# Kernel optimization log

Measured on AMD Instinct MI355X. Metric: run time of the kernel, lower is better.

Reference implementation:

```python
import jax, jax.numpy as jnp
from jax import lax
import numpy as np
import math

EPS = 1e-6

def _np(a, s=1.0):
    return np.asarray(a, dtype=np.float32) * np.float32(s)

def _gabor(theta, sigma=1.1, lambd=3.0, gamma=0.65):
    c = np.arange(-2, 3, dtype=np.float32)
    yy, xx = np.meshgrid(c, c, indexing='ij')
    xt = xx * math.cos(theta) + yy * math.sin(theta)
    yt = -xx * math.sin(theta) + yy * math.cos(theta)
    k = np.exp(-(xt**2 + gamma**2 * yt**2) / (2.0 * sigma**2)) * np.cos(2.0 * math.pi * xt / lambd)
    k = k - k.mean()
    return (k / max(np.abs(k).sum(), 1e-6)).astype(np.float32)

def _dct_like(u=2, v=2, size=5):
    c = np.arange(size, dtype=np.float32)
    yy, xx = np.meshgrid(c, c, indexing='ij')
    k = np.cos(math.pi*(2*xx+1)*u/(2*size)) * np.cos(math.pi*(2*yy+1)*v/(2*size))
    k = k - k.mean()
    return (k / max(np.abs(k).sum(), 1e-6)).astype(np.float32)

# stacked 3x3 stencils: laplacian, hess_xx, hess_yy, hess_xy, sobel_x, sobel_y, diag_main, diag_anti, checkerboard
_K3 = np.stack([
    _np([[0,1,0],[1,-4,1],[0,1,0]]),
    _np([[0,0,0],[1,-2,1],[0,0,0]]),
    _np([[0,1,0],[0,-2,0],[0,1,0]]),
    _np([[1,0,-1],[0,0,0],[-1,0,1]], 0.25),
    _np([[-1,0,1],[-2,0,2],[-1,0,1]], 0.125),
    _np([[-1,-2,-1],[0,0,0],[1,2,1]], 0.125),
    _np([[-2,-1,0],[-1,0,1],[0,1,2]], 0.125),
    _np([[0,1,2],[-1,0,1],[-2,-1,0]], 0.125),
    _np([[1,-1,1],[-1,1,-1],[1,-1,1]], 1.0/9.0),
])[:, None]

_Z5 = np.zeros((5,5), np.float32)

def _row5(vals):
    k = _Z5.copy(); k[2, :] = vals; return k

def _col5(vals):
    k = _Z5.copy(); k[:, 2] = vals; return k

# stacked 5x5 stencils: ha_second_h, ha_second_v, ha_green_h, ha_green_v, mhc_green, stripe_x, stripe_y, gabor45, gabor135, dct
_K5 = np.stack([
    _row5([-0.5, 0.0, 1.0, 0.0, -0.5]),
    _col5([-0.5, 0.0, 1.0, 0.0, -0.5]),
    _row5([-0.25, 0.5, 0.5, 0.5, -0.25]),
    _col5([-0.25, 0.5, 0.5, 0.5, -0.25]),
    _np([[0,0,-1,0,0],[0,0,2,0,0],[-1,2,4,2,-1],[0,0,2,0,0],[0,0,-1,0,0]], 0.125),
    _row5([0.25, -1.0, 1.5, -1.0, 0.25]),
    _col5([0.25, -1.0, 1.5, -1.0, 0.25]),
    _gabor(math.pi/4.0),
    _gabor(3.0*math.pi/4.0),
    _dct_like(),
])[:, None]

_SMOOTH5 = (_np([[1,2,3,2,1],[2,4,6,4,2],[3,6,9,6,3],[2,4,6,4,2],[1,2,3,2,1]]) / np.float32(81.0))[None, None]

K3 = jnp.asarray(_K3)
K5 = jnp.asarray(_K5)
SMOOTH5 = jnp.asarray(_SMOOTH5)

def _masks(H, W):
    # gbrg pattern
    z = lambda: np.zeros((1, 1, H, W), np.float32)
    r, b, gr, gb, row, col = z(), z(), z(), z(), z(), z()
    row[:, :, 1::2, :] = 1.0
    col[:, :, :, 1::2] = 1.0
    gb[:, :, 0::2, 0::2] = 1.0
    b[:, :, 0::2, 1::2] = 1.0
    r[:, :, 1::2, 0::2] = 1.0
    gr[:, :, 1::2, 1::2] = 1.0
    g = gr + gb
    return tuple(jnp.asarray(a) for a in (r, g, b, gr, gb, row, col))

def _pad(x, ph, pw):
    return jnp.pad(x, ((0, 0), (0, 0), (ph, ph), (pw, pw)), mode='reflect')

def _conv_same(x, k, groups=1):
    kh, kw = k.shape[-2:]
    return lax.conv_general_dilated(_pad(x, kh // 2, kw // 2), k.astype(x.dtype), (1, 1), 'VALID',
                                    dimension_numbers=('NCHW', 'OIHW', 'NCHW'),
                                    feature_group_count=groups)

def _avg_same(x, kh, kw):
    k = jnp.full((1, 1, kh, kw), 1.0 / (kh * kw), x.dtype)
    return _conv_same(x, k)

def _forward(bayer):
    B, _, H, W = bayer.shape
    r, g, b, gr, gb, row, col = _masks(H, W)
    c3 = _conv_same(bayer, K3)  # [B,9,H,W]
    lap, hxx, hyy, hxy, gx, gy, gdm, gda, chk = jnp.split(c3, 9, axis=1)
    c5 = _conv_same(bayer, K5)  # [B,10,H,W]
    hsh, hsv, hgh, hgv, mhcf, stx, sty, g45, g135, dctp = jnp.split(c5, 10, axis=1)
    # morphological gradient: 3x3 max - min (reflect-padded)
    xp = _pad(bayer, 1, 1)
    mgrad = (lax.reduce_window(xp, -jnp.inf, lax.max, (1, 1, 3, 3), (1, 1, 1, 1), 'VALID')
             - lax.reduce_window(xp, jnp.inf, lax.min, (1, 1, 3, 3), (1, 1, 1, 1), 'VALID'))
    gmag = jnp.sqrt(gx * gx + gy * gy + EPS)
    # structure tensor (3x3 box smoothing of gradient outer products)
    jxx = _avg_same(gx * gx, 3, 3)
    jyy = _avg_same(gy * gy, 3, 3)
    jxy = _avg_same(gx * gy, 3, 3)
    tr = jxx + jyy
    lam_gap = jnp.sqrt((jxx - jyy) ** 2 + 4.0 * jxy * jxy + EPS)
    coherence = lam_gap / (tr + EPS)
    anisotropy = (jxx - jyy) / (tr + EPS)
    ha_dis = jnp.abs(hgh - hgv)
    res_h = bayer - hgh
    res_v = bayer - hgv
    res_eh = _avg_same(res_h * res_h, 3, 3)
    res_ev = _avg_same(res_v * res_v, 3, 3)
    dgd = jnp.abs(gx) - jnp.abs(gy)
    dsd = jnp.abs(hxx) - jnp.abs(hyy)
    # 1x5 / 5x1 line variances
    mh = _avg_same(bayer, 1, 5)
    mv = _avg_same(bayer, 5, 1)
    lvh = jnp.maximum(_avg_same(bayer * bayer, 1, 5) - mh * mh, 0.0)
    lvv = jnp.maximum(_avg_same(bayer * bayer, 5, 1) - mv * mv, 0.0)
    lvd = lvh - lvv
    dconf = jnp.abs(lvd) / (lvh + lvv + EPS)
    # normalized sparse fills (smooth5 of masked signal / smooth5 of mask)
    mstack = jnp.concatenate([r, g, b, gr, gb], axis=1)  # [1,5,H,W]
    sig = bayer * mstack  # [B,5,H,W]
    ks = jnp.tile(SMOOTH5, (5, 1, 1, 1))
    num = _conv_same(sig, ks, groups=5)
    den = jnp.maximum(_conv_same(mstack, ks, groups=5), EPS)
    rf, gf, bf, grf, gbf = jnp.split(num / den, 5, axis=1)
    rg = rf - gf
    bg = bf - gf
    gpd = grf - gbf
    mhc = jnp.where(g > 0.5, bayer, mhcf)
    mhc_ha = mhc - 0.5 * (hgh + hgv)
    rres = (bayer - mhc) * r
    bres = (bayer - mhc) * b
    chk_e = _avg_same(chk * chk, 3, 3)
    str_e = _avg_same(stx * stx + sty * sty, 3, 3)
    lmean = _avg_same(bayer, 3, 3)
    lvar = jnp.maximum(_avg_same(bayer * bayer, 3, 3) - lmean * lmean, 0.0)
    gen = _avg_same(gx * gx + gy * gy, 3, 3)
    bm = lambda m: jnp.broadcast_to(m, bayer.shape)
    feats = [bm(r), bm(g), bm(b), bm(gr), bm(gb), bm(row), bm(col),
             lap, hxx, hyy, hxy, mgrad, gx, gy, gdm, gda, gmag,
             coherence, anisotropy, hsh, hsv, hgh, hgv, ha_dis,
             res_h, res_v, res_eh, res_ev, dgd, dsd, lvh, lvv, lvd, dconf,
             rg, bg, gpd, mhc, mhc_ha, rres, bres,
             stx, sty, chk, g45, g135, dctp, chk_e, str_e, lmean, lvar, gen]
    return jnp.concatenate(feats, axis=1)  # [B,52,H,W]

def setup_inputs() -> dict:
    key = jax.random.key(0)
    bayer = jax.random.uniform(key, (2, 1, 768, 768), dtype=jnp.float32)
    return {"bayer": bayer}

def reference(bayer):
    return _forward(bayer)
```

## Files before the change

### kernel.cpp

```cpp
#include <hip/hip_runtime.h>
#include <math.h>

#define H_ 768
#define W_ 768
#define TY 16
#define TX 64
#define NTHREADS 256
#define EPS_ 1e-6f

typedef float f4 __attribute__((ext_vector_type(4)));

__device__ __forceinline__ f4 mk4(float x, float y, float z, float w){ f4 r; r.x=x; r.y=y; r.z=z; r.w=w; return r; }
__device__ __forceinline__ f4 sp(float s){ return mk4(s,s,s,s); }
__device__ __forceinline__ f4 max4(f4 a, f4 b){ return mk4(fmaxf(a.x,b.x),fmaxf(a.y,b.y),fmaxf(a.z,b.z),fmaxf(a.w,b.w)); }
__device__ __forceinline__ f4 min4(f4 a, f4 b){ return mk4(fminf(a.x,b.x),fminf(a.y,b.y),fminf(a.z,b.z),fminf(a.w,b.w)); }
__device__ __forceinline__ f4 sqrt4(f4 a){ return mk4(sqrtf(a.x),sqrtf(a.y),sqrtf(a.z),sqrtf(a.w)); }
__device__ __forceinline__ f4 abs4(f4 a){ return mk4(fabsf(a.x),fabsf(a.y),fabsf(a.z),fabsf(a.w)); }
__device__ __forceinline__ float rcp1(float x){
#if __has_builtin(__builtin_amdgcn_rcpf)
    return __builtin_amdgcn_rcpf(x);
#else
    return 1.0f / x;
#endif
}
__device__ __forceinline__ f4 rcp4(f4 a){ return mk4(rcp1(a.x),rcp1(a.y),rcp1(a.z),rcp1(a.w)); }

__device__ __forceinline__ int refl(int c, int n) {
    c = c < 0 ? -c : c;
    return c >= n ? 2 * n - 2 - c : c;
}

__global__ __launch_bounds__(NTHREADS, 4)
void bayer_feat(const float* __restrict__ in, float* __restrict__ out) {
    const int bz  = blockIdx.z;
    const int gy0 = blockIdx.y * TY;
    const int gx0 = blockIdx.x * TX;
    const int tid = threadIdx.x;
    const float* src = in + (size_t)bz * (H_ * W_);

    __shared__ float sB[TY + 6][TX + 7];
    __shared__ float sE[7][TY + 2][TX + 3];

    for (int i = tid; i < (TY + 6) * (TX + 6); i += NTHREADS) {
        int r = i / (TX + 6), c = i - r * (TX + 6);
        sB[r][c] = src[refl(gy0 - 3 + r, H_) * W_ + refl(gx0 - 3 + c, W_)];
    }
    __syncthreads();

    for (int i = tid; i < (TY + 2) * (TX + 2); i += NTHREADS) {
        int ey = i / (TX + 2), ex = i - ey * (TX + 2);
        int sy = refl(gy0 - 1 + ey, H_) - gy0 + 3;
        int sx = refl(gx0 - 1 + ex, W_) - gx0 + 3;
        float a00 = sB[sy-1][sx-1], a01 = sB[sy-1][sx], a02 = sB[sy-1][sx+1];
        float a10 = sB[sy  ][sx-1], a11 = sB[sy  ][sx], a12 = sB[sy  ][sx+1];
        float a20 = sB[sy+1][sx-1], a21 = sB[sy+1][sx], a22 = sB[sy+1][sx+1];
        float l2 = sB[sy][sx-2], r2 = sB[sy][sx+2];
        float u2 = sB[sy-2][sx], d2 = sB[sy+2][sx];
        sE[0][ey][ex] = 0.125f * (-a00 + a02 - 2.f*a10 + 2.f*a12 - a20 + a22);
        sE[1][ey][ex] = 0.125f * (-a00 - 2.f*a01 - a02 + a20 + 2.f*a21 + a22);
        sE[2][ey][ex] = -0.25f*(l2 + r2) + 0.5f*(a10 + a11 + a12);
        sE[3][ey][ex] = -0.25f*(u2 + d2) + 0.5f*(a01 + a11 + a21);
        sE[4][ey][ex] = (a00 - a01 + a02 - a10 + a11 - a12 + a20 - a21 + a22) * (1.f/9.f);
        sE[5][ey][ex] = 0.25f*(l2 + r2) - (a10 + a12) + 1.5f*a11;
        sE[6][ey][ex] = 0.25f*(u2 + d2) - (a01 + a21) + 1.5f*a11;
    }
    __syncthreads();

    const int lq  = tid & 15;
    const int ly  = tid >> 4;
    const int lx4 = lq * 4;
    const int gy  = gy0 + ly;
    const int py  = gy & 1;
    const int syc = ly + 3;
    const int ey  = ly + 1;
    const int exb = lx4 + 1;
    const size_t HW = (size_t)H_ * W_;
    float* po = out + (size_t)bz * 52 * HW + (size_t)gy * W_ + (gx0 + lx4);

#define ST(c, v) *(f4*)(po + (size_t)(c) * HW) = (v)
#define AV(r, i) mk4(a[r][i], a[r][(i)+1], a[r][(i)+2], a[r][(i)+3])
#define SL(arr, o) mk4(arr[o], arr[(o)+1], arr[(o)+2], arr[(o)+3])
#define CTR(f) mk4(sE[f][ey][exb], sE[f][ey][exb+1], sE[f][ey][exb+2], sE[f][ey][exb+3])

    const f4 zero4 = sp(0.f);
    const f4 ev01  = mk4(0,1,0,1);
    const f4 ev10  = mk4(1,0,1,0);
    const float inv9 = 1.f / 9.f;

    float a[5][8];
#pragma unroll
    for (int r = 0; r < 5; ++r)
#pragma unroll
        for (int i = 0; i < 8; ++i)
            a[r][i] = sB[syc - 2 + r][lx4 + 1 + i];


    {
        const float G45[5][5] = {
            {-0.002092f, -0.015195f, -0.063321f, -0.002285f,  0.036511f},
            {-0.015195f, -0.086304f,  0.003803f,  0.119456f, -0.002285f},
            {-0.063321f,  0.003803f,  0.172851f,  0.003803f, -0.063321f},
            {-0.002285f,  0.119456f,  0.003803f, -0.086304f, -0.015195f},
            { 0.036511f, -0.002285f, -0.063321f, -0.015195f, -0.002092f}
        };
        const float ADC[5] = {0.25f, -0.09549150f, -0.30901699f, -0.09549150f, 0.25f};
        f4 s45 = zero4, s135 = zero4, dct = zero4;
#pragma unroll
        for (int r = 0; r < 5; ++r) {
            f4 t = zero4;
#pragma unroll
            for (int i = 0; i < 5; ++i) {
                f4 v = AV(r, i);
                s45  += sp(G45[r][i])     * v;
                s135 += sp(G45[r][4 - i]) * v;
                t    += sp(ADC[i])        * v;
            }
            dct += sp(ADC[r]) * t;
        }
        ST(44, s45); ST(45, s135); ST(46, dct);
    }

    {
        f4 t0 = zero4, t1 = zero4, t2 = zero4, t3 = zero4;
#pragma unroll
        for (int r = 0; r < 5; ++r) {
            f4 E = AV(r,0) + sp(3.f)*AV(r,2) + AV(r,4);
            f4 O = sp(2.f)*(AV(r,1) + AV(r,3));
            f4 rE = mk4(E.x, O.y, E.z, O.w);
            f4 rO = mk4(O.x, E.y, O.z, E.w);
            if (r == 0 || r == 4)      { t0 += rE;          t2 += rO; }
            else if (r == 2)           { t0 += sp(3.f)*rE;  t2 += sp(3.f)*rO; }
            else                       { t1 += sp(2.f)*rE;  t3 += sp(2.f)*rO; }
        }
        f4 cEE = py ? t1 : t0, cOE = py ? t0 : t1, cEO = py ? t3 : t2, cOO = py ? t2 : t3;
        const f4 inv_r  = py ? mk4(0.04f,0.05f,0.04f,0.05f)     : mk4(0.05f,0.0625f,0.05f,0.0625f);
        const f4 inv_b  = py ? mk4(0.0625f,0.05f,0.0625f,0.05f) : mk4(0.05f,0.04f,0.05f,0.04f);
        const f4 inv_gr = py ? mk4(0.05f,0.04f,0.05f,0.04f)     : mk4(0.0625f,0.05f,0.0625f,0.05f);
        const f4 inv_gb = py ? mk4(0.05f,0.0625f,0.05f,0.0625f) : mk4(0.04f,0.05f,0.04f,0.05f);
        const f4 inv_g  = py ? mk4(1.f/40.f,1.f/41.f,1.f/40.f,1.f/41.f)
                             : mk4(1.f/41.f,1.f/40.f,1.f/41.f,1.f/40.f);
        f4 rfv = cOE*inv_r, bfv = cEO*inv_b, grfv = cOO*inv_gr, gbfv = cEE*inv_gb;
        f4 gfv = (cEE + cOO)*inv_g;
        ST(34, rfv - gfv); ST(35, bfv - gfv); ST(36, grfv - gbfv);
    }

    f4 ctr = AV(2,2);

    {
        f4 sh = AV(2,0)+AV(2,1)+ctr+AV(2,3)+AV(2,4);
        f4 qh = AV(2,0)*AV(2,0)+AV(2,1)*AV(2,1)+ctr*ctr+AV(2,3)*AV(2,3)+AV(2,4)*AV(2,4);
        f4 sv_ = AV(0,2)+AV(1,2)+ctr+AV(3,2)+AV(4,2);
        f4 qv_ = AV(0,2)*AV(0,2)+AV(1,2)*AV(1,2)+ctr*ctr+AV(3,2)*AV(3,2)+AV(4,2)*AV(4,2);
        f4 mh = sh * sp(0.2f), mv = sv_ * sp(0.2f);
        f4 lvh = max4(qh*sp(0.2f) - mh*mh, zero4);
        f4 lvv = max4(qv_*sp(0.2f) - mv*mv, zero4);
        ST(30, lvh); ST(31, lvv);
        f4 lvd = lvh - lvv;
        ST(32, lvd);
        ST(33, abs4(lvd) * rcp4(lvh + lvv + sp(EPS_)));
    }

    ST(19, sp(-0.5f)*(AV(2,0) + AV(2,4)) + ctr);
    ST(20, sp(-0.5f)*(AV(0,2) + AV(4,2)) + ctr);

    f4 hghv = CTR(2), hgvv = CTR(3);
    {
        f4 mhcf = sp(0.125f)*( -AV(0,2) + sp(2.f)*AV(1,2) - AV(2,0) + sp(2.f)*AV(2,1) + sp(4.f)*ctr
                               + sp(2.f)*AV(2,3) - AV(2,4) + sp(2.f)*AV(3,2) - AV(4,2) );
        f4 mhc = py ? mk4(mhcf.x, ctr.y, mhcf.z, ctr.w) : mk4(ctr.x, mhcf.y, ctr.z, mhcf.w);
        ST(37, mhc);
        ST(38, mhc - sp(0.5f)*(hghv + hgvv));
        f4 dif = ctr - mhc;
        ST(39, dif * (py ? ev10 : zero4));
        ST(40, dif * (py ? zero4 : ev01));
    }
    ST(21, hghv); ST(22, hgvv);
    ST(23, abs4(hghv - hgvv));
    ST(24, ctr - hghv); ST(25, ctr - hgvv);

    {
        f4 lap = AV(1,2) + AV(2,1) - sp(4.f)*ctr + AV(2,3) + AV(3,2);
        f4 hxx = AV(2,1) - sp(2.f)*ctr + AV(2,3);
        f4 hyy = AV(1,2) - sp(2.f)*ctr + AV(3,2);
        f4 hxy = sp(0.25f)*(AV(1,1) - AV(1,3) - AV(3,1) + AV(3,3));
        ST(7, lap); ST(8, hxx); ST(9, hyy); ST(10, hxy);
        ST(29, abs4(hxx) - abs4(hyy));
    }
    ST(14, sp(0.125f)*(sp(-2.f)*AV(1,1) - AV(1,2) - AV(2,1) + AV(2,3) + AV(3,2) + sp(2.f)*AV(3,3)));
    ST(15, sp(0.125f)*(AV(1,2) + sp(2.f)*AV(1,3) - AV(2,1) + AV(2,3) - sp(2.f)*AV(3,1) - AV(3,2)));

    {
        f4 mx = AV(1,1), mn = mx, s3 = zero4, q3 = zero4;
#pragma unroll
        for (int r = 1; r <= 3; ++r)
#pragma unroll
            for (int i = 1; i <= 3; ++i) {
                f4 v = AV(r,i);
                mx = max4(mx, v); mn = min4(mn, v);
                s3 += v; q3 += v*v;
            }
        ST(11, mx - mn);
        f4 lmean = s3 * sp(inv9);
        ST(49, lmean);
        ST(50, max4(q3*sp(inv9) - lmean*lmean, zero4));
    }

    {
        f4 gxv = CTR(0), gyv = CTR(1);
        ST(12, gxv); ST(13, gyv);
        ST(16, sqrt4(gxv*gxv + gyv*gyv + sp(EPS_)));
        ST(28, abs4(gxv) - abs4(gyv));
    }
    ST(41, CTR(5)); ST(42, CTR(6)); ST(43, CTR(4));

    {
        f4 jxx = zero4, jyy = zero4, jxy = zero4, reh = zero4, rev = zero4, cke = zero4, ste = zero4;
#pragma unroll
        for (int dy = -1; dy <= 1; ++dy) {
            float g_[6], h_[6], hh_[6], hv_[6], ck_[6], sx_[6], sy_[6];
#pragma unroll
            for (int j = 0; j < 6; ++j) {
                g_[j]  = sE[0][ey+dy][exb-1+j];
                h_[j]  = sE[1][ey+dy][exb-1+j];
                hh_[j] = sE[2][ey+dy][exb-1+j];
                hv_[j] = sE[3][ey+dy][exb-1+j];
                ck_[j] = sE[4][ey+dy][exb-1+j];
                sx_[j] = sE[5][ey+dy][exb-1+j];
                sy_[j] = sE[6][ey+dy][exb-1+j];
            }
            f4 bm_ = AV(dy+2, 1), b0_ = AV(dy+2, 2), bp_ = AV(dy+2, 3);
#pragma unroll
            for (int o = 0; o < 3; ++o) {
                f4 q = SL(g_, o), w = SL(h_, o);
                jxx += q*q; jyy += w*w; jxy += q*w;
                f4 bb = (o == 0) ? bm_ : (o == 1 ? b0_ : bp_);
                f4 rh = bb - SL(hh_, o); reh += rh*rh;
                f4 rv = bb - SL(hv_, o); rev += rv*rv;
                f4 cc = SL(ck_, o); cke += cc*cc;
                f4 s1 = SL(sx_, o), s2 = SL(sy_, o);
                ste += s1*s1 + s2*s2;
            }
        }
        jxx = jxx * sp(inv9); jyy = jyy * sp(inv9); jxy = jxy * sp(inv9);
        f4 trc = jxx + jyy;
        f4 dj  = jxx - jyy;
        f4 lam = sqrt4(dj*dj + sp(4.f)*jxy*jxy + sp(EPS_));
        f4 itr = rcp4(trc + sp(EPS_));
        ST(17, lam * itr);
        ST(18, dj * itr);
        ST(51, trc);
        ST(26, reh * sp(inv9)); ST(27, rev * sp(inv9));
        ST(47, cke * sp(inv9)); ST(48, ste * sp(inv9));
    }

    ST(0, py ? ev10 : zero4);
    ST(1, py ? ev01 : ev10);
    ST(2, py ? zero4 : ev01);
    ST(3, py ? ev01 : zero4);
    ST(4, py ? zero4 : ev10);
    ST(5, sp((float)py));
    ST(6, ev01);

#undef ST
#undef AV
#undef SL
#undef CTR
}

extern "C" void kernel_launch(void* const* d_in, const int* in_sizes, int n_in,
                              void* d_out, int out_size, void* d_ws, size_t ws_size,
                              hipStream_t stream) {
    (void)n_in; (void)d_ws; (void)ws_size; (void)out_size;
    const float* bayer = (const float*)d_in[0];
    float* out = (float*)d_out;
    const int B = in_sizes[0] / (H_ * W_);
    dim3 grid(W_ / TX, H_ / TY, B);
    bayer_feat<<<grid, NTHREADS, 0, stream>>>(bayer, out);
}
```

Measured before the change: 46.09 us.

## Pack intermediate stencil products as fp16 pairs in LDS and halve tile size

```diff
diff --git a/kernel.cpp b/kernel.cpp
--- a/kernel.cpp
+++ b/kernel.cpp
@@ -3,17 +3,17 @@
 
 #define H_ 768
 #define W_ 768
-#define TY 16
+#define TY 8
 #define TX 64
-#define NTHREADS 256
+#define NTHREADS 128
 #define EPS_ 1e-6f
 
 typedef float f4 __attribute__((ext_vector_type(4)));
+typedef _Float16 h2 __attribute__((ext_vector_type(2)));
 
 __device__ __forceinline__ f4 mk4(float x, float y, float z, float w){ f4 r; r.x=x; r.y=y; r.z=z; r.w=w; return r; }
 __device__ __forceinline__ f4 sp(float s){ return mk4(s,s,s,s); }
 __device__ __forceinline__ f4 max4(f4 a, f4 b){ return mk4(fmaxf(a.x,b.x),fmaxf(a.y,b.y),fmaxf(a.z,b.z),fmaxf(a.w,b.w)); }
-__device__ __forceinline__ f4 min4(f4 a, f4 b){ return mk4(fminf(a.x,b.x),fminf(a.y,b.y),fminf(a.z,b.z),fminf(a.w,b.w)); }
 __device__ __forceinline__ f4 sqrt4(f4 a){ return mk4(sqrtf(a.x),sqrtf(a.y),sqrtf(a.z),sqrtf(a.w)); }
 __device__ __forceinline__ f4 abs4(f4 a){ return mk4(fabsf(a.x),fabsf(a.y),fabsf(a.z),fabsf(a.w)); }
 __device__ __forceinline__ float rcp1(float x){
@@ -24,6 +24,7 @@
 #endif
 }
 __device__ __forceinline__ f4 rcp4(f4 a){ return mk4(rcp1(a.x),rcp1(a.y),rcp1(a.z),rcp1(a.w)); }
+__device__ __forceinline__ h2 pk(float a, float b){ h2 r; r.x = (_Float16)a; r.y = (_Float16)b; return r; }
 
 __device__ __forceinline__ int refl(int c, int n) {
     c = c < 0 ? -c : c;
@@ -39,7 +40,7 @@
     const float* src = in + (size_t)bz * (H_ * W_);
 
     __shared__ float sB[TY + 6][TX + 7];
-    __shared__ float sE[7][TY + 2][TX + 3];
+    __shared__ h2 sP[3][TY + 2][TX + 3];
 
     for (int i = tid; i < (TY + 6) * (TX + 6); i += NTHREADS) {
         int r = i / (TX + 6), c = i - r * (TX + 6);
@@ -56,13 +57,17 @@
         float a20 = sB[sy+1][sx-1], a21 = sB[sy+1][sx], a22 = sB[sy+1][sx+1];
         float l2 = sB[sy][sx-2], r2 = sB[sy][sx+2];
         float u2 = sB[sy-2][sx], d2 = sB[sy+2][sx];
-        sE[0][ey][ex] = 0.125f * (-a00 + a02 - 2.f*a10 + 2.f*a12 - a20 + a22);
-        sE[1][ey][ex] = 0.125f * (-a00 - 2.f*a01 - a02 + a20 + 2.f*a21 + a22);
-        sE[2][ey][ex] = -0.25f*(l2 + r2) + 0.5f*(a10 + a11 + a12);
-        sE[3][ey][ex] = -0.25f*(u2 + d2) + 0.5f*(a01 + a11 + a21);
-        sE[4][ey][ex] = (a00 - a01 + a02 - a10 + a11 - a12 + a20 - a21 + a22) * (1.f/9.f);
-        sE[5][ey][ex] = 0.25f*(l2 + r2) - (a10 + a12) + 1.5f*a11;
-        sE[6][ey][ex] = 0.25f*(u2 + d2) - (a01 + a21) + 1.5f*a11;
+        float gx  = 0.125f * (-a00 + a02 - 2.f*a10 + 2.f*a12 - a20 + a22);
+        float gy  = 0.125f * (-a00 - 2.f*a01 - a02 + a20 + 2.f*a21 + a22);
+        float hgh = -0.25f*(l2 + r2) + 0.5f*(a10 + a11 + a12);
+        float hgv = -0.25f*(u2 + d2) + 0.5f*(a01 + a11 + a21);
+        float chk = (a00 - a01 + a02 - a10 + a11 - a12 + a20 - a21 + a22) * (1.f/9.f);
+        float stx = 0.25f*(l2 + r2) - (a10 + a12) + 1.5f*a11;
+        float sty = 0.25f*(u2 + d2) - (a01 + a21) + 1.5f*a11;
+        float rh = a11 - hgh, rv = a11 - hgv;
+        sP[0][ey][ex] = pk(gx, gy);
+        sP[1][ey][ex] = pk(rh*rh, rv*rv);
+        sP[2][ey][ex] = pk(chk*chk, stx*stx + sty*sty);
     }
     __syncthreads();
 
@@ -79,8 +84,6 @@
 
 #define ST(c, v) *(f4*)(po + (size_t)(c) * HW) = (v)
 #define AV(r, i) mk4(a[r][i], a[r][(i)+1], a[r][(i)+2], a[r][(i)+3])
-#define SL(arr, o) mk4(arr[o], arr[(o)+1], arr[(o)+2], arr[(o)+3])
-#define CTR(f) mk4(sE[f][ey][exb], sE[f][ey][exb+1], sE[f][ey][exb+2], sE[f][ey][exb+3])
 
     const f4 zero4 = sp(0.f);
     const f4 ev01  = mk4(0,1,0,1);
@@ -163,20 +166,35 @@
     ST(19, sp(-0.5f)*(AV(2,0) + AV(2,4)) + ctr);
     ST(20, sp(-0.5f)*(AV(0,2) + AV(4,2)) + ctr);
 
-    f4 hghv = CTR(2), hgvv = CTR(3);
+    f4 hghc = sp(-0.25f)*(AV(2,0) + AV(2,4)) + sp(0.5f)*(AV(2,1) + ctr + AV(2,3));
+    f4 hgvc = sp(-0.25f)*(AV(0,2) + AV(4,2)) + sp(0.5f)*(AV(1,2) + ctr + AV(3,2));
     {
         f4 mhcf = sp(0.125f)*( -AV(0,2) + sp(2.f)*AV(1,2) - AV(2,0) + sp(2.f)*AV(2,1) + sp(4.f)*ctr
                                + sp(2.f)*AV(2,3) - AV(2,4) + sp(2.f)*AV(3,2) - AV(4,2) );
         f4 mhc = py ? mk4(mhcf.x, ctr.y, mhcf.z, ctr.w) : mk4(ctr.x, mhcf.y, ctr.z, mhcf.w);
         ST(37, mhc);
-        ST(38, mhc - sp(0.5f)*(hghv + hgvv));
+        ST(38, mhc - sp(0.5f)*(hghc + hgvc));
         f4 dif = ctr - mhc;
         ST(39, dif * (py ? ev10 : zero4));
         ST(40, dif * (py ? zero4 : ev01));
     }
-    ST(21, hghv); ST(22, hgvv);
-    ST(23, abs4(hghv - hgvv));
-    ST(24, ctr - hghv); ST(25, ctr - hgvv);
+    ST(21, hghc); ST(22, hgvc);
+    ST(23, abs4(hghc - hgvc));
+    ST(24, ctr - hghc); ST(25, ctr - hgvc);
+
+    {
+        f4 gxc = sp(0.125f)*(-AV(1,1) + AV(1,3) - sp(2.f)*AV(2,1) + sp(2.f)*AV(2,3) - AV(3,1) + AV(3,3));
+        f4 gyc = sp(0.125f)*(-AV(1,1) - sp(2.f)*AV(1,2) - AV(1,3) + AV(3,1) + sp(2.f)*AV(3,2) + AV(3,3));
+        ST(12, gxc); ST(13, gyc);
+        ST(16, sqrt4(gxc*gxc + gyc*gyc + sp(EPS_)));
+        ST(28, abs4(gxc) - abs4(gyc));
+    }
+    {
+        f4 stxc = sp(0.25f)*(AV(2,0) + AV(2,4)) - (AV(2,1) + AV(2,3)) + sp(1.5f)*ctr;
+        f4 styc = sp(0.25f)*(AV(0,2) + AV(4,2)) - (AV(1,2) + AV(3,2)) + sp(1.5f)*ctr;
+        f4 chkc = (AV(1,1) - AV(1,2) + AV(1,3) - AV(2,1) + ctr - AV(2,3) + AV(3,1) - AV(3,2) + AV(3,3)) * sp(inv9);
+        ST(41, stxc); ST(42, styc); ST(43, chkc);
+    }
 
     {
         f4 lap = AV(1,2) + AV(2,1) - sp(4.f)*ctr + AV(2,3) + AV(3,2);
@@ -196,7 +214,8 @@
 #pragma unroll
             for (int i = 1; i <= 3; ++i) {
                 f4 v = AV(r,i);
-                mx = max4(mx, v); mn = min4(mn, v);
+                mx = max4(mx, v);
+                mn = mk4(fminf(mn.x,v.x),fminf(mn.y,v.y),fminf(mn.z,v.z),fminf(mn.w,v.w));
                 s3 += v; q3 += v*v;
             }
         ST(11, mx - mn);
@@ -206,39 +225,38 @@
     }
 
     {
-        f4 gxv = CTR(0), gyv = CTR(1);
-        ST(12, gxv); ST(13, gyv);
-        ST(16, sqrt4(gxv*gxv + gyv*gyv + sp(EPS_)));
-        ST(28, abs4(gxv) - abs4(gyv));
-    }
-    ST(41, CTR(5)); ST(42, CTR(6)); ST(43, CTR(4));
-
-    {
         f4 jxx = zero4, jyy = zero4, jxy = zero4, reh = zero4, rev = zero4, cke = zero4, ste = zero4;
 #pragma unroll
         for (int dy = -1; dy <= 1; ++dy) {
-            float g_[6], h_[6], hh_[6], hv_[6], ck_[6], sx_[6], sy_[6];
+            float g_[6], h_[6];
 #pragma unroll
             for (int j = 0; j < 6; ++j) {
-                g_[j]  = sE[0][ey+dy][exb-1+j];
-                h_[j]  = sE[1][ey+dy][exb-1+j];
-                hh_[j] = sE[2][ey+dy][exb-1+j];
-                hv_[j] = sE[3][ey+dy][exb-1+j];
-                ck_[j] = sE[4][ey+dy][exb-1+j];
-                sx_[j] = sE[5][ey+dy][exb-1+j];
-                sy_[j] = sE[6][ey+dy][exb-1+j];
-            }
-            f4 bm_ = AV(dy+2, 1), b0_ = AV(dy+2, 2), bp_ = AV(dy+2, 3);
+                h2 v0 = sP[0][ey+dy][exb-1+j];
+                g_[j] = (float)v0.x; h_[j] = (float)v0.y;
+                h2 v1 = sP[1][ey+dy][exb-1+j];
+                h2 v2 = sP[2][ey+dy][exb-1+j];
+                (void)v1; (void)v2;
+            }
 #pragma unroll
             for (int o = 0; o < 3; ++o) {
-                f4 q = SL(g_, o), w = SL(h_, o);
+                f4 q = mk4(g_[o], g_[o+1], g_[o+2], g_[o+3]);
+                f4 w = mk4(h_[o], h_[o+1], h_[o+2], h_[o+3]);
                 jxx += q*q; jyy += w*w; jxy += q*w;
-                f4 bb = (o == 0) ? bm_ : (o == 1 ? b0_ : bp_);
-                f4 rh = bb - SL(hh_, o); reh += rh*rh;
-                f4 rv = bb - SL(hv_, o); rev += rv*rv;
-                f4 cc = SL(ck_, o); cke += cc*cc;
-                f4 s1 = SL(sx_, o), s2 = SL(sy_, o);
-                ste += s1*s1 + s2*s2;
+            }
+            float r2_[6], v2_[6], c2_[6], ss_[6];
+#pragma unroll
+            for (int j = 0; j < 6; ++j) {
+                h2 v1 = sP[1][ey+dy][exb-1+j];
+                r2_[j] = (float)v1.x; v2_[j] = (float)v1.y;
+                h2 v2 = sP[2][ey+dy][exb-1+j];
+                c2_[j] = (float)v2.x; ss_[j] = (float)v2.y;
+            }
+#pragma unroll
+            for (int o = 0; o < 3; ++o) {
+                reh += mk4(r2_[o], r2_[o+1], r2_[o+2], r2_[o+3]);
+                rev += mk4(v2_[o], v2_[o+1], v2_[o+2], v2_[o+3]);
+                cke += mk4(c2_[o], c2_[o+1], c2_[o+2], c2_[o+3]);
+                ste += mk4(ss_[o], ss_[o+1], ss_[o+2], ss_[o+3]);
             }
         }
         jxx = jxx * sp(inv9); jyy = jyy * sp(inv9); jxy = jxy * sp(inv9);
@@ -263,8 +281,6 @@
 
 #undef ST
 #undef AV
-#undef SL
-#undef CTR
 }
 
 extern "C" void kernel_launch(void* const* d_in, const int* in_sizes, int n_in,
```

Measured after the change: 47.53 us. 3.1% more time.
